# Optimization experiments

Measured on AMD Instinct MI355X. Metric: run time of the kernel, lower is better.

The kernel has to match this reference:

```python
import jax, jax.numpy as jnp
import numpy as np

B, S, D, H = 4, 1024, 512, 8
DH = D // H
NEG = -1e32


def setup_inputs() -> dict:
    key = jax.random.key(0)
    ks = jax.random.split(key, 8)
    w_scale = (6.0 / (D + D)) ** 0.5  # xavier_uniform bound scale (approx, gaussian draw)
    def nrm(i, shape, scale=1.0):
        return jax.random.normal(ks[i], shape, jnp.float32) * scale
    return {
        "q": nrm(0, (B, S, D)),
        "k": nrm(1, (B, S, D)),
        "v": nrm(2, (B, S, D)),
        # causal lower-triangular mask (attend to self and past)
        "mask": jnp.tril(jnp.ones((1, 1, S, S), jnp.int32)),
        "Wq": nrm(3, (D, D), w_scale), "bq": jnp.zeros((D,), jnp.float32),
        "Wk": nrm(4, (D, D), w_scale), "bk": jnp.zeros((D,), jnp.float32),
        "Wv": nrm(5, (D, D), w_scale), "bv": jnp.zeros((D,), jnp.float32),
        "Wo": nrm(6, (D, D), w_scale), "bo": jnp.zeros((D,), jnp.float32),
        "gammas": nrm(7, (H, 1, 1), 0.5),
    }


def reference(q, k, v, mask, Wq, bq, Wk, bk, Wv, bv, Wo, bo, gammas):
    maskf = mask.astype(jnp.float32)
    neg = mask == 0

    def proj(x, W, b):
        # nn.Linear: x @ W.T + b, then split heads -> [B,H,S,DH]
        return (x @ W.T + b).reshape(B, S, H, DH).transpose(0, 2, 1, 3)

    qh, kh, vh = proj(q, Wq, bq), proj(k, Wk, bk), proj(v, Wv, bv)
    scores = jnp.einsum('bhqd,bhkd->bhqk', qh, kh) / jnp.sqrt(jnp.float32(DH))

    pos = jnp.arange(S, dtype=jnp.float32)
    position_effect = jnp.abs(pos[None, :] - pos[:, None])  # [S,S] = |i - j|

    # no-grad branch: masked softmax -> cumulative / total attention mass
    sm = jax.nn.softmax(jnp.where(neg, NEG, scores), axis=-1) * maskf
    distcum = jnp.cumsum(sm, axis=-1)
    disttotal = jnp.sum(sm, axis=-1, keepdims=True)
    dist_scores = jnp.sqrt(jnp.maximum((disttotal - distcum) * position_effect, 0.0))
    dist_scores = jax.lax.stop_gradient(dist_scores)

    gamma = -jax.nn.softplus(gammas)[None]  # [1,H,1,1], learned decay rate
    total_effect = jnp.clip(jnp.exp(dist_scores * gamma), 1e-5, 1e5)

    attn = jax.nn.softmax(jnp.where(neg, NEG, scores * total_effect), axis=-1)
    attn = attn.at[:, :, 0, :].set(0.0)  # zero_pad=True: zero out first query row
    # dropout is identity at eval time

    out = jnp.einsum('bhqk,bhkd->bhqd', attn, vh)
    concat = out.transpose(0, 2, 1, 3).reshape(B, S, D)
    output = concat @ Wo.T + bo
    return output, attn
```

## Files before the change

### kernel.cpp

```cpp
#include <hip/hip_runtime.h>
#include <hip/hip_bf16.h>

typedef __attribute__((ext_vector_type(8))) _Float16 half8;
typedef __attribute__((ext_vector_type(4))) _Float16 half4v;
typedef __attribute__((ext_vector_type(4))) float f32x4;

#define MFMA16(a, b, c) __builtin_amdgcn_mfma_f32_16x16x32_f16((a), (b), (c), 0, 0, 0)

static constexpr int Bb = 4, Ss = 1024, Dd = 512, Hh = 8, DHh = 64;
static constexpr float LOG2E = 1.44269504f;
static constexpr float FNEG = -65504.f;

__device__ __forceinline__ half4v f2h4(float4 f) {
  half4v h;
  h[0] = (_Float16)f.x; h[1] = (_Float16)f.y;
  h[2] = (_Float16)f.z; h[3] = (_Float16)f.w;
  return h;
}

template<int MODE>
__global__ __launch_bounds__(256) void gemm_k(
    const void* A0v, const void* A1v, const float* Bm0, const float* Bm1,
    const float* bias0, const float* bias1, void* C0v, void* C1v,
    int M, int N, int K)
{
  __shared__ _Float16 As[128 * 72];
  __shared__ _Float16 Bs[64 * 72];

  const int tid = threadIdx.x;
  const int w = tid >> 6, l = tid & 63;
  const int wr = w >> 1, wc = w & 1;
  const int l4 = l >> 4, lm = l & 15;
  const int m0 = blockIdx.x * 128, n0 = blockIdx.y * 64;
  const int z = (MODE == 0) ? (int)blockIdx.z : 0;

  const float* Af = (const float*)(z ? A1v : A0v);
  const ushort* Ab = (const ushort*)A0v;
  const float* Bw = z ? Bm1 : Bm0;
  const float* bias = z ? bias1 : bias0;

  f32x4 zz = {0.f, 0.f, 0.f, 0.f};
  f32x4 acc[4][2];
#pragma unroll
  for (int i2 = 0; i2 < 4; ++i2)
#pragma unroll
    for (int j = 0; j < 2; ++j) acc[i2][j] = zz;

  for (int k0 = 0; k0 < K; k0 += 64) {
#pragma unroll
    for (int it = 0; it < 8; ++it) {
      int f4 = it * 256 + tid;
      int rowi = f4 >> 4, c4 = (f4 & 15) << 2;
      if constexpr (MODE == 1) {
        ushort4 u = *(const ushort4*)&Ab[(size_t)(m0 + rowi) * K + k0 + c4];
        *(ushort4*)&As[rowi * 72 + c4] = u;
      } else {
        float4 f = *(const float4*)&Af[(size_t)(m0 + rowi) * K + k0 + c4];
        *(half4v*)&As[rowi * 72 + c4] = f2h4(f);
      }
    }
#pragma unroll
    for (int it = 0; it < 4; ++it) {
      int f4 = it * 256 + tid;
      int rowi = f4 >> 4, c4 = (f4 & 15) << 2;
      float4 f = *(const float4*)&Bw[(size_t)(n0 + rowi) * K + k0 + c4];
      *(half4v*)&Bs[rowi * 72 + c4] = f2h4(f);
    }
    __syncthreads();
#pragma unroll
    for (int ks = 0; ks < 2; ++ks) {
      half8 a[4], b[2];
#pragma unroll
      for (int mf = 0; mf < 4; ++mf)
        a[mf] = *(const half8*)&As[(wr * 64 + mf * 16 + lm) * 72 + ks * 32 + l4 * 8];
#pragma unroll
      for (int nf = 0; nf < 2; ++nf)
        b[nf] = *(const half8*)&Bs[(wc * 32 + nf * 16 + lm) * 72 + ks * 32 + l4 * 8];
#pragma unroll
      for (int mf = 0; mf < 4; ++mf)
#pragma unroll
        for (int nf = 0; nf < 2; ++nf)
          acc[mf][nf] = MFMA16(a[mf], b[nf], acc[mf][nf]);
    }
    __syncthreads();
  }

  _Float16* Ch = (_Float16*)(z ? C1v : C0v);
  float* Cf = (float*)C0v;
#pragma unroll
  for (int mf = 0; mf < 4; ++mf) {
#pragma unroll
    for (int nf = 0; nf < 2; ++nf) {
      int row0 = m0 + wr * 64 + mf * 16 + l4 * 4;
      int col = n0 + wc * 32 + nf * 16 + lm;
      f32x4 vv = acc[mf][nf];
#pragma unroll
      for (int r = 0; r < 4; ++r) {
        int row = row0 + r;
        float val = vv[r];
        if constexpr (MODE == 0) {
          val += bias[col];
          int idx = (((row >> 10) * Hh + (col >> 6)) * Ss + (row & 1023)) * DHh + (col & 63);
          Ch[idx] = (_Float16)val;
        } else if constexpr (MODE == 2) {
          val += bias[row];
          int idx = (((col >> 10) * Hh + (row >> 6)) * DHh + (row & 63)) * Ss + (col & 1023);
          Ch[idx] = (_Float16)val;
        } else {
          val += bias[col];
          Cf[(size_t)row * N + col] = val;
        }
      }
    }
  }
}

__global__ __launch_bounds__(512, 4) void attn_k(
    const _Float16* __restrict__ qh, const _Float16* __restrict__ kh,
    const _Float16* __restrict__ vT, const float* __restrict__ gammas,
    float* __restrict__ attn_out, _Float16* __restrict__ concat)
{
  constexpr int TW = 1064;
  __shared__ __align__(16) _Float16 tile[32 * TW];
  __shared__ float invZ[32];

  const int tid = threadIdx.x;
  const int w = tid >> 6, l = tid & 63;
  const int l4 = l >> 4, lm = l & 15;
  const int bh = blockIdx.y;
  const int b = bh >> 3, h = bh & 7;

  const float g = gammas[h];
  const float g2 = -log1pf(__expf(g)) * LOG2E;
  constexpr float SC2 = 0.125f * LOG2E;

  f32x4 zz = {0.f, 0.f, 0.f, 0.f};

  for (int half = 0; half < 2; ++half) {
    const int qr0 = half ? (Ss - 32 - blockIdx.x * 32) : (blockIdx.x * 32);
    const int nvalid = qr0 + 32;
    __syncthreads();

    const _Float16* Qp = qh + ((size_t)bh * Ss + qr0) * DHh;
    const _Float16* Kp = kh + (size_t)bh * Ss * DHh;

    {
      const int NF = nvalid >> 4;
      const int NFpad = ((nvalid + 63) & ~63) >> 4;
      half8 aq[2][2];
#pragma unroll
      for (int mf = 0; mf < 2; ++mf)
#pragma unroll
        for (int ks = 0; ks < 2; ++ks)
          aq[mf][ks] = *(const half8*)&Qp[(mf * 16 + lm) * DHh + ks * 32 + l4 * 8];

      float pmr[2][4], pt0[2][4];
#pragma unroll
      for (int mf = 0; mf < 2; ++mf)
#pragma unroll
        for (int r = 0; r < 4; ++r) { pmr[mf][r] = -3.0e38f; pt0[mf][r] = 0.f; }

      for (int f = w; f < NFpad; f += 8) {
        f32x4 acc[2] = {zz, zz};
        const bool live = (f < NF);
        if (live) {
#pragma unroll
          for (int ks = 0; ks < 2; ++ks) {
            half8 bb = *(const half8*)&Kp[(size_t)(f * 16 + lm) * DHh + ks * 32 + l4 * 8];
            acc[0] = MFMA16(aq[0][ks], bb, acc[0]);
            acc[1] = MFMA16(aq[1][ks], bb, acc[1]);
          }
        }
        const int colc = f * 16 + lm;
#pragma unroll
        for (int mf = 0; mf < 2; ++mf)
#pragma unroll
          for (int r = 0; r < 4; ++r) {
            const int rg = mf * 16 + l4 * 4 + r;
            float val = (live && colc <= qr0 + rg) ? acc[mf][r] * SC2 : FNEG;
            _Float16 vh = (_Float16)val;
            tile[rg * TW + colc] = vh;
            float vf = (float)vh;
            pmr[mf][r] = fmaxf(pmr[mf][r], vf);
            pt0[mf][r] += exp2f(vf);
          }
      }
#pragma unroll
      for (int d = 1; d < 16; d <<= 1)
#pragma unroll
        for (int mf = 0; mf < 2; ++mf)
#pragma unroll
          for (int r = 0; r < 4; ++r) {
            pmr[mf][r] = fmaxf(pmr[mf][r], __shfl_xor(pmr[mf][r], d, 16));
            pt0[mf][r] += __shfl_xor(pt0[mf][r], d, 16);
          }
      if (lm == 0) {
#pragma unroll
        for (int mf = 0; mf < 2; ++mf)
#pragma unroll
          for (int r = 0; r < 4; ++r) {
            const int rg = mf * 16 + l4 * 4 + r;
            float* sp = (float*)&tile[rg * TW + 1024];
            sp[w] = pmr[mf][r];
            sp[8 + w] = pt0[mf][r];
          }
      }
    }
    __syncthreads();

    {
      const int rr = tid >> 4, t16 = tid & 15;
      const int i = qr0 + rr;
      const int nch = (i >> 6) + 1;
      _Float16* row = tile + rr * TW;
      const float* sp = (const float*)&row[1024];

      float mx = sp[0];
      float T0 = sp[8];
#pragma unroll
      for (int ww = 1; ww < 8; ++ww) {
        mx = fmaxf(mx, sp[ww]);
        T0 += sp[8 + ww];
      }
      const float invT0 = 1.f / T0;
      const float Msh = fmaxf(mx, 0.f);

      float carry = 0.f, Z2 = 0.f;
      for (int c = 0; c < nch; ++c) {
        const int col = (c << 6) + (t16 << 2);
        half4v s4 = *(const half4v*)&row[col];
        float s[4], e[4];
#pragma unroll
        for (int j = 0; j < 4; ++j) {
          s[j] = (float)s4[j];
          e[j] = exp2f(s[j]);
        }
        const float lsum = (e[0] + e[1]) + (e[2] + e[3]);
        float sc = lsum;
#pragma unroll
        for (int d = 1; d < 16; d <<= 1) {
          float o = __shfl_up(sc, d, 16);
          if (t16 >= d) sc += o;
        }
        float run = carry + (sc - lsum);
        carry += __shfl(sc, 15, 16);
        const float dj = (float)(i - col);
        half4v u4;
#pragma unroll
        for (int j = 0; j < 4; ++j) {
          run += e[j];
          float prod = fmaxf((T0 - run) * invT0 * (dj - (float)j), 0.f);
          float eff = fmaxf(exp2f(g2 * sqrtf(prod)), 1e-5f);
          float uu = exp2f(s[j] * eff - Msh);
          Z2 += uu;
          u4[j] = (_Float16)uu;
        }
        *(half4v*)&row[col] = u4;
      }
#pragma unroll
      for (int d = 8; d; d >>= 1) Z2 += __shfl_xor(Z2, d, 16);
      const float invZ2v = (i == 0) ? 0.f : 1.f / Z2;
      if (t16 == 0) invZ[rr] = invZ2v;

      float* arow = attn_out + ((size_t)bh * Ss + i) * Ss;
      for (int c = 0; c < Ss / 64; ++c) {
        const int col = (c << 6) + (t16 << 2);
        float4 pv = {0.f, 0.f, 0.f, 0.f};
        if (c < nch) {
          half4v u4 = *(const half4v*)&row[col];
          float* pp = (float*)&pv;
#pragma unroll
          for (int j = 0; j < 4; ++j) pp[j] = (float)u4[j] * invZ2v;
        }
        *(float4*)&arow[col] = pv;
      }
    }
    __syncthreads();

    f32x4 acc2[2][4];
#pragma unroll
    for (int mf = 0; mf < 2; ++mf)
#pragma unroll
      for (int nf = 0; nf < 4; ++nf) acc2[mf][nf] = zz;
    {
      const int NC = nvalid >> 5;
      const _Float16* Vp = vT + (size_t)bh * DHh * Ss;
      for (int c = w; c < NC; c += 8) {
        const int kb = c << 5;
        half8 pa[2];
#pragma unroll
        for (int mf = 0; mf < 2; ++mf)
          pa[mf] = *(const half8*)&tile[(mf * 16 + lm) * TW + kb + l4 * 8];
#pragma unroll
        for (int nf = 0; nf < 4; ++nf) {
          half8 bb = *(const half8*)&Vp[(size_t)(nf * 16 + lm) * Ss + kb + l4 * 8];
          acc2[0][nf] = MFMA16(pa[0], bb, acc2[0][nf]);
          acc2[1][nf] = MFMA16(pa[1], bb, acc2[1][nf]);
        }
      }
    }
    __syncthreads();
    float* pps = (float*)tile;
#pragma unroll
    for (int mf = 0; mf < 2; ++mf)
#pragma unroll
      for (int nf = 0; nf < 4; ++nf)
#pragma unroll
        for (int r = 0; r < 4; ++r)
          pps[w * 2048 + (mf * 16 + l4 * 4 + r) * 64 + nf * 16 + lm] = acc2[mf][nf][r];
    __syncthreads();
    for (int idx = tid; idx < 2048; idx += 512) {
      int mr = idx >> 6, nc = idx & 63;
      float ssum = 0.f;
#pragma unroll
      for (int ww = 0; ww < 8; ++ww) ssum += pps[ww * 2048 + idx];
      concat[((size_t)(b * Ss + qr0 + mr)) * Dd + h * DHh + nc] =
          (_Float16)(ssum * invZ[mr]);
    }
  }
}

extern "C" void kernel_launch(void* const* d_in, const int* in_sizes, int n_in,
                              void* d_out, int out_size, void* d_ws, size_t ws_size,
                              hipStream_t stream) {
  const float* q  = (const float*)d_in[0];
  const float* k  = (const float*)d_in[1];
  const float* v  = (const float*)d_in[2];
  const float* Wq = (const float*)d_in[4];
  const float* bq = (const float*)d_in[5];
  const float* Wk = (const float*)d_in[6];
  const float* bk = (const float*)d_in[7];
  const float* Wv = (const float*)d_in[8];
  const float* bv = (const float*)d_in[9];
  const float* Wo = (const float*)d_in[10];
  const float* bo = (const float*)d_in[11];
  const float* gm = (const float*)d_in[12];

  _Float16* qhb = (_Float16*)d_ws;
  _Float16* khb = qhb + 2097152;
  _Float16* vT  = khb + 2097152;
  _Float16* cc  = vT  + 2097152;

  float* out  = (float*)d_out;
  float* attn = out + (size_t)Bb * Ss * Dd;

  gemm_k<0><<<dim3(32, 8, 2), 256, 0, stream>>>(q, k, Wq, Wk, bq, bk, qhb, khb,
                                                4096, 512, 512);
  gemm_k<2><<<dim3(4, 64, 1), 256, 0, stream>>>(Wv, nullptr, v, nullptr, bv, nullptr,
                                                vT, nullptr, 512, 4096, 512);
  attn_k<<<dim3(16, 32), 512, 0, stream>>>(qhb, khb, vT, gm, attn, cc);
  gemm_k<1><<<dim3(32, 8, 1), 256, 0, stream>>>(cc, nullptr, Wo, nullptr, bo, nullptr,
                                                out, nullptr, 4096, 512, 512);
}
```

Measured before the change: 102.7 us.

## Halve attention query tile to 16 rows with 256-thread blocks and double grid

Shrinks each attention block from 32 query rows / 8 waves to 16 query rows / 4 waves, doubling the grid to 1024 blocks and cutting shared memory per block roughly in half. The aim is more resident blocks per CU and better load balance across the causal triangle. In exchange, each K/V fragment loaded from global memory now feeds one MFMA row tile instead of two, so operand reuse drops and global K/V traffic rises.

```diff
diff --git a/kernel.cpp b/kernel.cpp
--- a/kernel.cpp
+++ b/kernel.cpp
@@ -115,14 +115,14 @@
   }
 }
 
-__global__ __launch_bounds__(512, 4) void attn_k(
+__global__ __launch_bounds__(256, 4) void attn_k(
     const _Float16* __restrict__ qh, const _Float16* __restrict__ kh,
     const _Float16* __restrict__ vT, const float* __restrict__ gammas,
     float* __restrict__ attn_out, _Float16* __restrict__ concat)
 {
-  constexpr int TW = 1064;
-  __shared__ __align__(16) _Float16 tile[32 * TW];
-  __shared__ float invZ[32];
+  constexpr int TW = 1048;
+  __shared__ __align__(16) _Float16 tile[16 * TW];
+  __shared__ float invZ[16];
 
   const int tid = threadIdx.x;
   const int w = tid >> 6, l = tid & 63;
@@ -137,8 +137,8 @@
   f32x4 zz = {0.f, 0.f, 0.f, 0.f};
 
   for (int half = 0; half < 2; ++half) {
-    const int qr0 = half ? (Ss - 32 - blockIdx.x * 32) : (blockIdx.x * 32);
-    const int nvalid = qr0 + 32;
+    const int qr0 = half ? (1008 - blockIdx.x * 16) : (blockIdx.x * 16);
+    const int nvalid = qr0 + 16;
     __syncthreads();
 
     const _Float16* Qp = qh + ((size_t)bh * Ss + qr0) * DHh;
@@ -147,63 +147,52 @@
     {
       const int NF = nvalid >> 4;
       const int NFpad = ((nvalid + 63) & ~63) >> 4;
-      half8 aq[2][2];
-#pragma unroll
-      for (int mf = 0; mf < 2; ++mf)
-#pragma unroll
-        for (int ks = 0; ks < 2; ++ks)
-          aq[mf][ks] = *(const half8*)&Qp[(mf * 16 + lm) * DHh + ks * 32 + l4 * 8];
-
-      float pmr[2][4], pt0[2][4];
-#pragma unroll
-      for (int mf = 0; mf < 2; ++mf)
-#pragma unroll
-        for (int r = 0; r < 4; ++r) { pmr[mf][r] = -3.0e38f; pt0[mf][r] = 0.f; }
-
-      for (int f = w; f < NFpad; f += 8) {
-        f32x4 acc[2] = {zz, zz};
+      half8 aq[2];
+#pragma unroll
+      for (int ks = 0; ks < 2; ++ks)
+        aq[ks] = *(const half8*)&Qp[lm * DHh + ks * 32 + l4 * 8];
+
+      float pmr[4], pt0[4];
+#pragma unroll
+      for (int r = 0; r < 4; ++r) { pmr[r] = -3.0e38f; pt0[r] = 0.f; }
+
+      for (int f = w; f < NFpad; f += 4) {
+        f32x4 acc = zz;
         const bool live = (f < NF);
         if (live) {
 #pragma unroll
           for (int ks = 0; ks < 2; ++ks) {
             half8 bb = *(const half8*)&Kp[(size_t)(f * 16 + lm) * DHh + ks * 32 + l4 * 8];
-            acc[0] = MFMA16(aq[0][ks], bb, acc[0]);
-            acc[1] = MFMA16(aq[1][ks], bb, acc[1]);
+            acc = MFMA16(aq[ks], bb, acc);
           }
         }
         const int colc = f * 16 + lm;
 #pragma unroll
-        for (int mf = 0; mf < 2; ++mf)
-#pragma unroll
-          for (int r = 0; r < 4; ++r) {
-            const int rg = mf * 16 + l4 * 4 + r;
-            float val = (live && colc <= qr0 + rg) ? acc[mf][r] * SC2 : FNEG;
-            _Float16 vh = (_Float16)val;
-            tile[rg * TW + colc] = vh;
-            float vf = (float)vh;
-            pmr[mf][r] = fmaxf(pmr[mf][r], vf);
-            pt0[mf][r] += exp2f(vf);
-          }
+        for (int r = 0; r < 4; ++r) {
+          const int rg = l4 * 4 + r;
+          float val = (live && colc <= qr0 + rg) ? acc[r] * SC2 : FNEG;
+          _Float16 vh = (_Float16)val;
+          tile[rg * TW + colc] = vh;
+          float vf = (float)vh;
+          pmr[r] = fmaxf(pmr[r], vf);
+          pt0[r] += exp2f(vf);
+        }
       }
 #pragma unroll
       for (int d = 1; d < 16; d <<= 1)
 #pragma unroll
-        for (int mf = 0; mf < 2; ++mf)
-#pragma unroll
-          for (int r = 0; r < 4; ++r) {
-            pmr[mf][r] = fmaxf(pmr[mf][r], __shfl_xor(pmr[mf][r], d, 16));
-            pt0[mf][r] += __shfl_xor(pt0[mf][r], d, 16);
-          }
+        for (int r = 0; r < 4; ++r) {
+          pmr[r] = fmaxf(pmr[r], __shfl_xor(pmr[r], d, 16));
+          pt0[r] += __shfl_xor(pt0[r], d, 16);
+        }
       if (lm == 0) {
 #pragma unroll
-        for (int mf = 0; mf < 2; ++mf)
-#pragma unroll
-          for (int r = 0; r < 4; ++r) {
-            const int rg = mf * 16 + l4 * 4 + r;
-            float* sp = (float*)&tile[rg * TW + 1024];
-            sp[w] = pmr[mf][r];
-            sp[8 + w] = pt0[mf][r];
-          }
+        for (int r = 0; r < 4; ++r) {
+          const int rg = l4 * 4 + r;
+          float* sp = (float*)&tile[rg * TW + 1024];
+          sp[w] = pmr[r];
+          sp[4 + w] = pt0[r];
+        }
       }
     }
     __syncthreads();
@@ -215,13 +204,8 @@
       _Float16* row = tile + rr * TW;
       const float* sp = (const float*)&row[1024];
 
-      float mx = sp[0];
-      float T0 = sp[8];
-#pragma unroll
-      for (int ww = 1; ww < 8; ++ww) {
-        mx = fmaxf(mx, sp[ww]);
-        T0 += sp[8 + ww];
-      }
+      float mx = fmaxf(fmaxf(sp[0], sp[1]), fmaxf(sp[2], sp[3]));
+      float T0 = (sp[4] + sp[5]) + (sp[6] + sp[7]);
       const float invT0 = 1.f / T0;
       const float Msh = fmaxf(mx, 0.f);
 
@@ -277,43 +261,34 @@
     }
     __syncthreads();
 
-    f32x4 acc2[2][4];
-#pragma unroll
-    for (int mf = 0; mf < 2; ++mf)
-#pragma unroll
-      for (int nf = 0; nf < 4; ++nf) acc2[mf][nf] = zz;
+    f32x4 acc2[4];
+#pragma unroll
+    for (int nf = 0; nf < 4; ++nf) acc2[nf] = zz;
     {
-      const int NC = nvalid >> 5;
+      const int NC = (nvalid + 31) >> 5;
       const _Float16* Vp = vT + (size_t)bh * DHh * Ss;
-      for (int c = w; c < NC; c += 8) {
+      for (int c = w; c < NC; c += 4) {
         const int kb = c << 5;
-        half8 pa[2];
-#pragma unroll
-        for (int mf = 0; mf < 2; ++mf)
-          pa[mf] = *(const half8*)&tile[(mf * 16 + lm) * TW + kb + l4 * 8];
+        half8 pa = *(const half8*)&tile[lm * TW + kb + l4 * 8];
 #pragma unroll
         for (int nf = 0; nf < 4; ++nf) {
           half8 bb = *(const half8*)&Vp[(size_t)(nf * 16 + lm) * Ss + kb + l4 * 8];
-          acc2[0][nf] = MFMA16(pa[0], bb, acc2[0][nf]);
-          acc2[1][nf] = MFMA16(pa[1], bb, acc2[1][nf]);
+          acc2[nf] = MFMA16(pa, bb, acc2[nf]);
         }
       }
     }
     __syncthreads();
     float* pps = (float*)tile;
 #pragma unroll
-    for (int mf = 0; mf < 2; ++mf)
-#pragma unroll
-      for (int nf = 0; nf < 4; ++nf)
-#pragma unroll
-        for (int r = 0; r < 4; ++r)
-          pps[w * 2048 + (mf * 16 + l4 * 4 + r) * 64 + nf * 16 + lm] = acc2[mf][nf][r];
-    __syncthreads();
-    for (int idx = tid; idx < 2048; idx += 512) {
+    for (int nf = 0; nf < 4; ++nf)
+#pragma unroll
+      for (int r = 0; r < 4; ++r)
+        pps[w * 1024 + (l4 * 4 + r) * 64 + nf * 16 + lm] = acc2[nf][r];
+    __syncthreads();
+    for (int idx = tid; idx < 1024; idx += 256) {
       int mr = idx >> 6, nc = idx & 63;
-      float ssum = 0.f;
-#pragma unroll
-      for (int ww = 0; ww < 8; ++ww) ssum += pps[ww * 2048 + idx];
+      float ssum = ((pps[idx] + pps[1024 + idx]) +
+                    (pps[2048 + idx] + pps[3072 + idx]));
       concat[((size_t)(b * Ss + qr0 + mr)) * Dd + h * DHh + nc] =
           (_Float16)(ssum * invZ[mr]);
     }
@@ -348,7 +323,7 @@
                                                 4096, 512, 512);
   gemm_k<2><<<dim3(4, 64, 1), 256, 0, stream>>>(Wv, nullptr, v, nullptr, bv, nullptr,
                                                 vT, nullptr, 512, 4096, 512);
-  attn_k<<<dim3(16, 32), 512, 0, stream>>>(qhb, khb, vT, gm, attn, cc);
+  attn_k<<<dim3(32, 32), 256, 0, stream>>>(qhb, khb, vT, gm, attn, cc);
   gemm_k<1><<<dim3(32, 8, 1), 256, 0, stream>>>(cc, nullptr, Wo, nullptr, bo, nullptr,
                                                 out, nullptr, 4096, 512, 512);
 }
```

Result: slower. 106.4 us (+3.6%).

## Overlap attn-probability stores with PV MMA via warp specialization

Applied to the files above, without the earlier changes.

The PV product and the write-out of normalized attention probabilities now run on different warps. Four warps each compute a 16x32 output slice over the full key range and write concat directly. The other four warps stream the fp32 attention rows to global memory at the same time. This drops the cross-warp reduction through shared memory and its extra barriers, and hides the large attention-matrix store behind the MFMA work. In exchange, fewer warps share the MFMA work, so each does a longer serial loop, and the store traffic is carried by only half the block.

```diff
diff --git a/kernel.cpp b/kernel.cpp
--- a/kernel.cpp
+++ b/kernel.cpp
@@ -259,64 +259,55 @@
       }
 #pragma unroll
       for (int d = 8; d; d >>= 1) Z2 += __shfl_xor(Z2, d, 16);
-      const float invZ2v = (i == 0) ? 0.f : 1.f / Z2;
-      if (t16 == 0) invZ[rr] = invZ2v;
-
+      if (t16 == 0) invZ[rr] = (i == 0) ? 0.f : 1.f / Z2;
+    }
+    __syncthreads();
+
+    if (w < 4) {
+      const int rows0 = (w & 1) * 16;
+      const int dh0 = (w >> 1) * 32;
+      const _Float16* Vp = vT + (size_t)bh * DHh * Ss;
+      f32x4 acc2[2] = {zz, zz};
+      const int NC = (nvalid + 31) >> 5;
+      for (int c = 0; c < NC; ++c) {
+        const int kb = c << 5;
+        half8 pa = *(const half8*)&tile[(rows0 + lm) * TW + kb + l4 * 8];
+#pragma unroll
+        for (int nf = 0; nf < 2; ++nf) {
+          half8 bb = *(const half8*)&Vp[(size_t)(dh0 + nf * 16 + lm) * Ss + kb + l4 * 8];
+          acc2[nf] = MFMA16(pa, bb, acc2[nf]);
+        }
+      }
+#pragma unroll
+      for (int nf = 0; nf < 2; ++nf)
+#pragma unroll
+        for (int r = 0; r < 4; ++r) {
+          const int rg = rows0 + l4 * 4 + r;
+          concat[((size_t)(b * Ss + qr0 + rg)) * Dd + h * DHh + dh0 + nf * 16 + lm] =
+              (_Float16)(acc2[nf][r] * invZ[rg]);
+        }
+    } else {
+      const int gl = (w - 4) * 64 + l;
+      const int row = gl >> 3;
+      const int ln8 = gl & 7;
+      const int i = qr0 + row;
+      const float invZv = invZ[row];
+      const int climit = ((i >> 6) + 1) << 1;
+      const _Float16* urow = tile + row * TW;
       float* arow = attn_out + ((size_t)bh * Ss + i) * Ss;
-      for (int c = 0; c < Ss / 64; ++c) {
-        const int col = (c << 6) + (t16 << 2);
+      for (int c = 0; c < 32; ++c) {
+        const int col = (c << 5) + (ln8 << 2);
         float4 pv = {0.f, 0.f, 0.f, 0.f};
-        if (c < nch) {
-          half4v u4 = *(const half4v*)&row[col];
+        if (c < climit) {
+          half4v u4 = *(const half4v*)&urow[col];
           float* pp = (float*)&pv;
 #pragma unroll
-          for (int j = 0; j < 4; ++j) pp[j] = (float)u4[j] * invZ2v;
+          for (int j = 0; j < 4; ++j) pp[j] = (float)u4[j] * invZv;
         }
         *(float4*)&arow[col] = pv;
       }
     }
     __syncthreads();
-
-    f32x4 acc2[2][4];
-#pragma unroll
-    for (int mf = 0; mf < 2; ++mf)
-#pragma unroll
-      for (int nf = 0; nf < 4; ++nf) acc2[mf][nf] = zz;
-    {
-      const int NC = nvalid >> 5;
-      const _Float16* Vp = vT + (size_t)bh * DHh * Ss;
-      for (int c = w; c < NC; c += 8) {
-        const int kb = c << 5;
-        half8 pa[2];
-#pragma unroll
-        for (int mf = 0; mf < 2; ++mf)
-          pa[mf] = *(const half8*)&tile[(mf * 16 + lm) * TW + kb + l4 * 8];
-#pragma unroll
-        for (int nf = 0; nf < 4; ++nf) {
-          half8 bb = *(const half8*)&Vp[(size_t)(nf * 16 + lm) * Ss + kb + l4 * 8];
-          acc2[0][nf] = MFMA16(pa[0], bb, acc2[0][nf]);
-          acc2[1][nf] = MFMA16(pa[1], bb, acc2[1][nf]);
-        }
-      }
-    }
-    __syncthreads();
-    float* pps = (float*)tile;
-#pragma unroll
-    for (int mf = 0; mf < 2; ++mf)
-#pragma unroll
-      for (int nf = 0; nf < 4; ++nf)
-#pragma unroll
-        for (int r = 0; r < 4; ++r)
-          pps[w * 2048 + (mf * 16 + l4 * 4 + r) * 64 + nf * 16 + lm] = acc2[mf][nf][r];
-    __syncthreads();
-    for (int idx = tid; idx < 2048; idx += 512) {
-      int mr = idx >> 6, nc = idx & 63;
-      float ssum = 0.f;
-#pragma unroll
-      for (int ww = 0; ww < 8; ++ww) ssum += pps[ww * 2048 + idx];
-      concat[((size_t)(b * Ss + qr0 + mr)) * Dd + h * DHh + nc] =
-          (_Float16)(ssum * invZ[mr]);
-    }
   }
 }
 
```

Result: slower. 108.0 us (+5.1%).
